# Kernel tuning notes

Measured on AMD Instinct MI355X. Metric: run time of the kernel, lower is better.

## Reference

```python
import math
import jax, jax.numpy as jnp
import numpy as np

CAPACITY = 2097152  # 2**21, power of two -> complete sum tree
SIZE = 1048576


def _build_tree(probs):
    # Tree layout: node i has children 2i+1, 2i+2; leaves are tree[-capacity:].
    # For power-of-two capacity this is levels concatenated root-first.
    levels = [probs]
    x = probs
    while x.shape[0] > 1:
        x = x.reshape(-1, 2).sum(axis=1)
        levels.append(x)
    return jnp.concatenate(levels[::-1])


def setup_inputs() -> dict:
    key = jax.random.key(0)
    k1, k2 = jax.random.split(key)
    priorities = jax.random.uniform(k1, (CAPACITY,), dtype=jnp.float32)
    uniform = jax.random.uniform(k2, (SIZE,), dtype=jnp.float32)
    return {"priorities": priorities, "uniform": uniform, "size": SIZE}


def reference(priorities, uniform, size):
    cap = priorities.shape[0]
    depth = int(math.log2(cap))  # number of traversal steps (complete tree)
    tree = _build_tree(priorities)  # [2*cap - 1]
    total = tree[0]

    # sample() with equal_mode=True: stratified samples in [0, total)
    offsets = jnp.linspace(0.0, total, size + 1, dtype=jnp.float32)[:-1]
    sums = uniform * total / size + offsets  # [size]
    idx0 = jnp.zeros((size,), dtype=jnp.int32)

    def body(_, carry):
        idx, s = carry
        left = 2 * idx + 1
        left_val = tree[left]            # gather [size]
        go_left = s <= left_val
        idx = jnp.where(go_left, left, left + 1)
        s = jnp.where(go_left, s, s - left_val)
        return idx, s

    idx, _ = jax.lax.fori_loop(0, depth, body, (idx0, sums))
    return idx - cap + 1  # leaf index in [0, cap)
```

## Files before the change

kernel.cpp:

```cpp
#include <hip/hip_runtime.h>


#define CAP    (1 << 21)
#define NSAMP  (1 << 20)
#define L18OFF ((1 << 18) - 1)

__global__ __launch_bounds__(256) void build_tree(const float* __restrict__ prio,
                                                  float* __restrict__ tree) {
    __shared__ __align__(16) float A[512];
    __shared__ __align__(16) float B[256];
    const int b = blockIdx.x, t = threadIdx.x;
    const float4* p4 = (const float4*)(prio + (size_t)b * 4096);

    #pragma unroll
    for (int i = t; i < 512; i += 256) {
        float4 x = p4[2 * i], y = p4[2 * i + 1];
        A[i] = ((x.x + x.y) + (x.z + x.w)) + ((y.x + y.y) + (y.z + y.w));
    }
    __syncthreads();
    {
        float* g = tree + L18OFF + b * 512;
        #pragma unroll
        for (int i = t; i < 512; i += 256) g[i] = A[i];
    }
    float* src = A;
    float* dst = B;
    int cnt = 256;
    int off = (1 << 17) - 1;
    for (int lvl = 17; lvl >= 9; --lvl) {
        for (int i = t; i < cnt; i += 256) {
            float2 v = ((const float2*)src)[i];
            float r = v.x + v.y;
            dst[i] = r;
            tree[off + b * cnt + i] = r;
        }
        __syncthreads();
        float* tmp = src; src = dst; dst = tmp;
        off = (off - 1) >> 1;
        cnt >>= 1;
    }
}

__global__ __launch_bounds__(256) void sample_kernel(const float* __restrict__ tree,
                                                     const float* __restrict__ prio,
                                                     const float* __restrict__ uniform,
                                                     int* __restrict__ out) {
    __shared__ float nds[8191];
    const int t = threadIdx.x;

    for (int i = 511 + t; i < 8191; i += 256) nds[i] = tree[i];
    __syncthreads();
    {
        int cnt = 256, off = 255;
        for (int lvl = 8; lvl >= 0; --lvl) {
            for (int i = t; i < cnt; i += 256) {
                int n = off + i;
                nds[n] = nds[2 * n + 1] + nds[2 * n + 2];
            }
            __syncthreads();
            off = (off - 1) >> 1;
            cnt >>= 1;
        }
    }

    const float total = nds[0];
    const float scale = total / (float)NSAMP;
    const int base = blockIdx.x * 1024 + t;

    float s[4];
    int   id[4];
    #pragma unroll
    for (int q = 0; q < 4; ++q) {
        int j = base + 256 * q;
        s[q]  = uniform[j] * total / (float)NSAMP + scale * (float)j;
        id[q] = 0;
    }

    #pragma unroll
    for (int d = 0; d < 12; ++d) {
        #pragma unroll
        for (int q = 0; q < 4; ++q) {
            int left = 2 * id[q] + 1;
            float lv = nds[left];
            bool r = s[q] > lv;
            s[q]  = r ? s[q] - lv : s[q];
            id[q] = r ? left + 1 : left;
        }
    }
    #pragma unroll
    for (int d = 0; d < 6; ++d) {
        #pragma unroll
        for (int q = 0; q < 4; ++q) {
            int left = 2 * id[q] + 1;
            float lv = tree[left];
            bool r = s[q] > lv;
            s[q]  = r ? s[q] - lv : s[q];
            id[q] = r ? left + 1 : left;
        }
    }
    #pragma unroll
    for (int q = 0; q < 4; ++q) {
        int p = id[q] - L18OFF;
        const float4* pp = (const float4*)prio + 2 * (size_t)p;
        float4 x = pp[0], y = pp[1];
        float l19 = (x.x + x.y) + (x.z + x.w);
        bool r1 = s[q] > l19;
        float ss = r1 ? s[q] - l19 : s[q];
        float l20 = r1 ? (y.x + y.y) : (x.x + x.y);
        bool r2 = ss > l20;
        ss = r2 ? ss - l20 : ss;
        float leaf = r1 ? (r2 ? y.z : y.x) : (r2 ? x.z : x.x);
        bool r3 = ss > leaf;
        out[base + 256 * q] = 8 * p + (r1 ? 4 : 0) + (r2 ? 2 : 0) + (r3 ? 1 : 0);
    }
}

extern "C" void kernel_launch(void* const* d_in, const int* in_sizes, int n_in,
                              void* d_out, int out_size, void* d_ws, size_t ws_size,
                              hipStream_t stream) {
    const float* prio    = (const float*)d_in[0];
    const float* uniform = (const float*)d_in[1];
    (void)in_sizes; (void)n_in; (void)out_size; (void)ws_size;

    float* tree = (float*)d_ws;

    build_tree<<<512, 256, 0, stream>>>(prio, tree);
    sample_kernel<<<NSAMP / 1024, 256, 0, stream>>>(tree, prio, uniform, (int*)d_out);
}
```

Baseline: 76.32 us.

## Pack tree levels into 3-level treelet records for vectorized traversal

The build kernel now reduces each block fully in shared memory and writes only the upper levels plus compact 8-float treelet records, each covering three tree levels (13-15 and 16-18). The sampler replaces six dependent scattered global gathers with two pairs of float4 loads per sample and resolves three levels per load in registers. It also assigns consecutive samples to each thread so that uniform loads and output stores become 16-byte vectorized accesses. The cost is a more intricate index mapping and some wasted padding in each record.

```diff
diff --git a/kernel.cpp b/kernel.cpp
--- a/kernel.cpp
+++ b/kernel.cpp
@@ -4,51 +4,65 @@
 #define CAP    (1 << 21)
 #define NSAMP  (1 << 20)
 #define L18OFF ((1 << 18) - 1)
+#define AUX0_F 8192
+#define AUX1_F 40960
 
 __global__ __launch_bounds__(256) void build_tree(const float* __restrict__ prio,
-                                                  float* __restrict__ tree) {
-    __shared__ __align__(16) float A[512];
-    __shared__ __align__(16) float B[256];
+                                                  float* __restrict__ ws) {
+    __shared__ __align__(16) float H[1023];
     const int b = blockIdx.x, t = threadIdx.x;
     const float4* p4 = (const float4*)(prio + (size_t)b * 4096);
 
     #pragma unroll
     for (int i = t; i < 512; i += 256) {
         float4 x = p4[2 * i], y = p4[2 * i + 1];
-        A[i] = ((x.x + x.y) + (x.z + x.w)) + ((y.x + y.y) + (y.z + y.w));
+        H[511 + i] = ((x.x + x.y) + (x.z + x.w)) + ((y.x + y.y) + (y.z + y.w));
     }
     __syncthreads();
-    {
-        float* g = tree + L18OFF + b * 512;
-        #pragma unroll
-        for (int i = t; i < 512; i += 256) g[i] = A[i];
-    }
-    float* src = A;
-    float* dst = B;
-    int cnt = 256;
-    int off = (1 << 17) - 1;
-    for (int lvl = 17; lvl >= 9; --lvl) {
+    for (int cnt = 256, off = 255; cnt >= 1; off >>= 1, cnt >>= 1) {
         for (int i = t; i < cnt; i += 256) {
-            float2 v = ((const float2*)src)[i];
-            float r = v.x + v.y;
-            dst[i] = r;
-            tree[off + b * cnt + i] = r;
+            int h = off + i;
+            H[h] = H[2 * h + 1] + H[2 * h + 2];
         }
         __syncthreads();
-        float* tmp = src; src = dst; dst = tmp;
-        off = (off - 1) >> 1;
-        cnt >>= 1;
+    }
+
+    if (t == 0)  ws[511 + b] = H[0];
+    if (t < 2)   ws[1023 + 2 * b + t] = H[1 + t];
+    if (t < 4)   ws[2047 + 4 * b + t] = H[3 + t];
+    if (t < 8)   ws[4095 + 8 * b + t] = H[7 + t];
+
+    if (t < 64) {
+        int e = t >> 3, k = t & 7, h = 7 + e;
+        float v;
+        if      (k == 0) v = H[2 * h + 1];
+        else if (k == 1) v = H[4 * h + 3];
+        else if (k == 2) v = H[4 * h + 5];
+        else if (k <  7) v = H[8 * h + 7 + 2 * (k - 3)];
+        else             v = 0.0f;
+        ws[AUX0_F + (size_t)b * 64 + t] = v;
+    }
+    #pragma unroll
+    for (int i = t; i < 512; i += 256) {
+        int e = i >> 3, k = i & 7, h = 63 + e;
+        float v;
+        if      (k == 0) v = H[2 * h + 1];
+        else if (k == 1) v = H[4 * h + 3];
+        else if (k == 2) v = H[4 * h + 5];
+        else if (k <  7) v = H[8 * h + 7 + 2 * (k - 3)];
+        else             v = 0.0f;
+        ws[AUX1_F + (size_t)b * 512 + i] = v;
     }
 }
 
-__global__ __launch_bounds__(256) void sample_kernel(const float* __restrict__ tree,
+__global__ __launch_bounds__(256) void sample_kernel(const float* __restrict__ ws,
                                                      const float* __restrict__ prio,
                                                      const float* __restrict__ uniform,
                                                      int* __restrict__ out) {
     __shared__ float nds[8191];
     const int t = threadIdx.x;
 
-    for (int i = 511 + t; i < 8191; i += 256) nds[i] = tree[i];
+    for (int i = 511 + t; i < 8191; i += 256) nds[i] = ws[i];
     __syncthreads();
     {
         int cnt = 256, off = 255;
@@ -65,14 +79,17 @@
 
     const float total = nds[0];
     const float scale = total / (float)NSAMP;
-    const int base = blockIdx.x * 1024 + t;
+    const int j0 = blockIdx.x * 1024 + t * 4;
+
+    float4 u4 = *(const float4*)(uniform + j0);
+    float uu[4] = {u4.x, u4.y, u4.z, u4.w};
 
     float s[4];
     int   id[4];
     #pragma unroll
     for (int q = 0; q < 4; ++q) {
-        int j = base + 256 * q;
-        s[q]  = uniform[j] * total / (float)NSAMP + scale * (float)j;
+        int j = j0 + q;
+        s[q]  = uu[q] * total / (float)NSAMP + scale * (float)j;
         id[q] = 0;
     }
 
@@ -87,17 +104,53 @@
             id[q] = r ? left + 1 : left;
         }
     }
-    #pragma unroll
-    for (int d = 0; d < 6; ++d) {
+
+    {
+        float4 A0[4], A1[4];
         #pragma unroll
         for (int q = 0; q < 4; ++q) {
-            int left = 2 * id[q] + 1;
-            float lv = tree[left];
-            bool r = s[q] > lv;
-            s[q]  = r ? s[q] - lv : s[q];
-            id[q] = r ? left + 1 : left;
+            int l12 = id[q] - 4095;
+            const float4* a = (const float4*)(ws + AUX0_F + (size_t)l12 * 8);
+            A0[q] = a[0]; A1[q] = a[1];
+        }
+        #pragma unroll
+        for (int q = 0; q < 4; ++q) {
+            float ss = s[q];
+            float v13 = A0[q].x;
+            bool b0 = ss > v13; ss = b0 ? ss - v13 : ss;
+            float v14 = b0 ? A0[q].z : A0[q].y;
+            bool b1 = ss > v14; ss = b1 ? ss - v14 : ss;
+            float v15 = b1 ? (b0 ? A1[q].z : A1[q].x)
+                           : (b0 ? A1[q].y : A0[q].w);
+            bool b2 = ss > v15; ss = b2 ? ss - v15 : ss;
+            s[q]  = ss;
+            id[q] = 8 * id[q] + 7 + (b0 ? 4 : 0) + (b1 ? 2 : 0) + (b2 ? 1 : 0);
         }
     }
+    {
+        float4 A0[4], A1[4];
+        #pragma unroll
+        for (int q = 0; q < 4; ++q) {
+            int l15 = id[q] - 32767;
+            const float4* a = (const float4*)(ws + AUX1_F + (size_t)l15 * 8);
+            A0[q] = a[0]; A1[q] = a[1];
+        }
+        #pragma unroll
+        for (int q = 0; q < 4; ++q) {
+            float ss = s[q];
+            float v16 = A0[q].x;
+            bool b0 = ss > v16; ss = b0 ? ss - v16 : ss;
+            float v17 = b0 ? A0[q].z : A0[q].y;
+            bool b1 = ss > v17; ss = b1 ? ss - v17 : ss;
+            float v18 = b1 ? (b0 ? A1[q].z : A1[q].x)
+                           : (b0 ? A1[q].y : A0[q].w);
+            bool b2 = ss > v18; ss = b2 ? ss - v18 : ss;
+            s[q]  = ss;
+            id[q] = 8 * id[q] + 7 + (b0 ? 4 : 0) + (b1 ? 2 : 0) + (b2 ? 1 : 0);
+        }
+    }
+
+    int res[4];
     #pragma unroll
     for (int q = 0; q < 4; ++q) {
         int p = id[q] - L18OFF;
@@ -111,8 +164,9 @@
         ss = r2 ? ss - l20 : ss;
         float leaf = r1 ? (r2 ? y.z : y.x) : (r2 ? x.z : x.x);
         bool r3 = ss > leaf;
-        out[base + 256 * q] = 8 * p + (r1 ? 4 : 0) + (r2 ? 2 : 0) + (r3 ? 1 : 0);
+        res[q] = 8 * p + (r1 ? 4 : 0) + (r2 ? 2 : 0) + (r3 ? 1 : 0);
     }
+    *(int4*)(out + j0) = make_int4(res[0], res[1], res[2], res[3]);
 }
 
 extern "C" void kernel_launch(void* const* d_in, const int* in_sizes, int n_in,
@@ -122,8 +176,8 @@
     const float* uniform = (const float*)d_in[1];
     (void)in_sizes; (void)n_in; (void)out_size; (void)ws_size;
 
-    float* tree = (float*)d_ws;
+    float* ws = (float*)d_ws;
 
-    build_tree<<<512, 256, 0, stream>>>(prio, tree);
-    sample_kernel<<<NSAMP / 1024, 256, 0, stream>>>(tree, prio, uniform, (int*)d_out);
+    build_tree<<<512, 256, 0, stream>>>(prio, ws);
+    sample_kernel<<<NSAMP / 1024, 256, 0, stream>>>(ws, prio, uniform, (int*)d_out);
 }
```

After: 75.90 us. About the same (-0.6%).
